# Optimization experiments

Measured on AMD Instinct MI355X. Metric: run time of the kernel, lower is better.

## Reference

```python
import math
import jax, jax.numpy as jnp
import numpy as np

N_HEADS = 16   # matches init_kwargs n_heads
C_SAMPLING = 1  # matches init_kwargs c_sampling


def setup_inputs() -> dict:
    rng = jax.random.key(0)
    ks = jax.random.split(rng, 8)
    L = S = 2048
    B = 8
    D = 1024
    sc = 0.02  # weight scale
    return {
        "query": jax.random.normal(ks[0], (L, B, D), jnp.float32),
        "key": jax.random.normal(ks[1], (S, B, D), jnp.float32),
        "value": jax.random.normal(ks[2], (S, B, D), jnp.float32),
        "Wq": jax.random.normal(ks[3], (D, D), jnp.float32) * sc,
        "bq": jnp.zeros((D,), jnp.float32),
        "Wk": jax.random.normal(ks[4], (D, D), jnp.float32) * sc,
        "bk": jnp.zeros((D,), jnp.float32),
        "Wv": jax.random.normal(ks[5], (D, D), jnp.float32) * sc,
        "bv": jnp.zeros((D,), jnp.float32),
        "Wo": jax.random.normal(ks[6], (D, D), jnp.float32) * sc,
        "bo": jnp.zeros((D,), jnp.float32),
    }


def _autocorr_forward(query, key, value, Wq, bq, Wk, bk, Wv, bv, Wo, bo):
    L, B, D = query.shape
    S = key.shape[0]
    H = N_HEADS
    E = D // H

    def proj(x, W, b):
        return x @ W.T + b

    def to_attn(x):  # (T,B,D) -> (B,H,E,T)
        T = x.shape[0]
        return x.reshape(T, B, H, E).transpose(1, 2, 3, 0)

    Q = to_attn(proj(query, Wq, bq))   # (B,H,E,L)
    K = to_attn(proj(key, Wk, bk))     # (B,H,E,S)
    V = to_attn(proj(value, Wv, bv))   # (B,H,E,S)

    # Align K/V length to L (static shapes: branch resolved at trace time)
    if L > S:
        pad = [(0, 0)] * 3 + [(0, L - S)]
        K = jnp.pad(K, pad)
        V = jnp.pad(V, pad)
    else:
        K = K[..., :L]
        V = V[..., :L]

    # Cross-correlation via FFT along time axis
    Qf = jnp.fft.rfft(Q, axis=-1)
    Kf = jnp.fft.rfft(K, axis=-1)
    corr = jnp.fft.irfft(Qf * jnp.conj(Kf), n=L, axis=-1)  # (B,H,E,L)

    # --- time_delay_agg ---
    topk = int(C_SAMPLING * math.log(L))
    mean_corr = corr.mean(axis=-2)                         # (B,H,L)
    scores, taus = jax.lax.top_k(mean_corr, topk)          # (B,H,topk)
    w = jax.nn.softmax(scores, axis=-1)                    # (B,H,topk)
    # delayed index (s + tau) mod L : (B,H,L,topk)
    idx = (jnp.arange(L)[None, None, :, None] + taus[:, :, None, :]) % L
    # gather V along time: (B,H,E,L,topk)
    delayed = jnp.take_along_axis(V[:, :, :, :, None], idx[:, :, None, :, :], axis=3)
    agg = jnp.mean(delayed * w[:, :, None, None, :], axis=-1)  # (B,H,E,L)

    # recover_from_attn: (B,H,E,L) -> (L,B,H*E)
    out = agg.transpose(3, 0, 1, 2).reshape(L, B, H * E)
    return out @ Wo.T + bo  # (L,B,D); need_weights=False so corr is dropped


def reference(query, key, value, Wq, bq, Wk, bk, Wv, bv, Wo, bo):
    return _autocorr_forward(query, key, value, Wq, bq, Wk, bk, Wv, bv, Wo, bo)
```

## Files before the change

### kernel.cpp

```cpp
#include <hip/hip_runtime.h>
#include <math.h>

#define TOPK 7

typedef __attribute__((ext_vector_type(8))) short bf16x8;
typedef __attribute__((ext_vector_type(4))) float f32x4;

__device__ __forceinline__ void glds16(const ushort* g, ushort* l)
{
    __builtin_amdgcn_global_load_lds(
        (const __attribute__((address_space(1))) void*)g,
        (__attribute__((address_space(3))) void*)l, 16, 0, 0);
}

__device__ __forceinline__ void split1(float x, ushort& h, ushort& lo)
{
    union U { float f; unsigned u; };
    U a; a.f = x;
    unsigned r = (a.u + 0x7FFFu + ((a.u >> 16) & 1u)) >> 16;
    h = (ushort)r;
    U b; b.u = r << 16;
    U d; d.f = x - b.f;
    unsigned r2 = (d.u + 0x7FFFu + ((d.u >> 16) & 1u)) >> 16;
    lo = (ushort)r2;
}

__global__ __launch_bounds__(256)
void split_f32(const float* __restrict__ x, ushort* __restrict__ hi,
               ushort* __restrict__ lo, int n4)
{
    for (int i = blockIdx.x * 256 + threadIdx.x; i < n4; i += gridDim.x * 256) {
        float4 v = ((const float4*)x)[i];
        ushort4 h, lw;
        split1(v.x, h.x, lw.x);
        split1(v.y, h.y, lw.y);
        split1(v.z, h.z, lw.z);
        split1(v.w, h.w, lw.w);
        ((ushort4*)hi)[i] = h;
        ((ushort4*)lo)[i] = lw;
    }
}

__global__ __launch_bounds__(256)
void wsplit4(const float* __restrict__ w0, const float* __restrict__ w1,
             const float* __restrict__ w2, const float* __restrict__ w3,
             ushort* __restrict__ o0, ushort* __restrict__ o1,
             ushort* __restrict__ o2, ushort* __restrict__ o3)
{
    const int m = blockIdx.x >> 10;
    const int lb = blockIdx.x & 1023;
    const float* src = (m == 0) ? w0 : (m == 1) ? w1 : (m == 2) ? w2 : w3;
    ushort* hi = (m == 0) ? o0 : (m == 1) ? o1 : (m == 2) ? o2 : o3;
    ushort* lo = hi + 1048576;
    const int n4 = 262144;
    for (int i = lb * 256 + threadIdx.x; i < n4; i += 1024 * 256) {
        float4 v = ((const float4*)src)[i];
        ushort4 h, lw;
        split1(v.x, h.x, lw.x);
        split1(v.y, h.y, lw.y);
        split1(v.z, h.z, lw.z);
        split1(v.w, h.w, lw.w);
        ((ushort4*)hi)[i] = h;
        ((ushort4*)lo)[i] = lw;
    }
}

template<bool TRANSP>
__global__ __launch_bounds__(512, 2)
void gemm_split(const ushort* __restrict__ Ah, const ushort* __restrict__ Al,
                const ushort* __restrict__ Bh, const ushort* __restrict__ Bl,
                const float* __restrict__ bias, float* __restrict__ C)
{
    __shared__ ushort lds[65536];
    const int tid = threadIdx.x;
    const int w = tid >> 6, l = tid & 63;

    const int ord = blockIdx.y * gridDim.x + blockIdx.x;
    const int cpx = (gridDim.x * gridDim.y) >> 3;
    const int swzb = (ord & 7) * cpx + (ord >> 3);
    const int bx = swzb & 3;
    const int by = swzb >> 2;

    const int wm = w >> 2, wn = w & 3;
    const int lr = l & 15, kgr = l >> 4;

    const ushort* gbB[4]; size_t goB[4]; int loB[4];
    const ushort* gbA[4]; size_t goA[4]; int loA[4];
#pragma unroll
    for (int q = 0; q < 4; ++q) {
        int idx = w * 4 + q;
        int cbq = idx >> 4;
        int kg = (idx >> 2) & 3;
        int rblk = idx & 3;
        gbB[q] = cbq ? Bl : Bh;
        goB[q] = (size_t)(bx * 256 + rblk * 64 + l) * 1024 + kg * 8;
        loB[q] = 16384 + cbq * 8192 + kg * 2048 + rblk * 512;
        gbA[q] = cbq ? Al : Ah;
        goA[q] = (size_t)(by * 256 + rblk * 64 + l) * 1024 + kg * 8;
        loA[q] = cbq * 8192 + kg * 2048 + rblk * 512;
    }

    f32x4 acc[8][4];
#pragma unroll
    for (int i = 0; i < 8; ++i)
#pragma unroll
        for (int j = 0; j < 4; ++j) acc[i][j] = (f32x4){0.f, 0.f, 0.f, 0.f};

#define STAGE_B(bufbase_, k0_) do { \
    const int _bb = (bufbase_); const int _kk = (k0_); \
    _Pragma("unroll") \
    for (int q = 0; q < 4; ++q) \
        glds16(gbB[q] + goB[q] + _kk, &lds[_bb + loB[q]]); \
} while (0)

#define STAGE_A2(bufbase_, k0_, qa_, qb_) do { \
    const int _bb = (bufbase_); const int _kk = (k0_); \
    glds16(gbA[qa_] + goA[qa_] + _kk, &lds[_bb + loA[qa_]]); \
    glds16(gbA[qb_] + goA[qb_] + _kk, &lds[_bb + loA[qb_]]); \
} while (0)

#define COMPUTE2(i0_) do { \
    _Pragma("unroll") \
    for (int ii = 0; ii < 2; ++ii) { \
        const int i = (i0_) + ii; \
        const int ra = wm * 128 + i * 16 + lr; \
        bf16x8 fah = *(const bf16x8*)&lb[       kgr * 2048 + ra * 8]; \
        bf16x8 fal = *(const bf16x8*)&lb[8192 + kgr * 2048 + ra * 8]; \
        __builtin_amdgcn_s_setprio(1); \
        _Pragma("unroll") \
        for (int j = 0; j < 4; ++j) \
            acc[i][j] = __builtin_amdgcn_mfma_f32_16x16x32_bf16(fah, fbh[j], acc[i][j], 0, 0, 0); \
        _Pragma("unroll") \
        for (int j = 0; j < 4; ++j) \
            acc[i][j] = __builtin_amdgcn_mfma_f32_16x16x32_bf16(fah, fbl[j], acc[i][j], 0, 0, 0); \
        _Pragma("unroll") \
        for (int j = 0; j < 4; ++j) \
            acc[i][j] = __builtin_amdgcn_mfma_f32_16x16x32_bf16(fal, fbh[j], acc[i][j], 0, 0, 0); \
        __builtin_amdgcn_s_setprio(0); \
    } \
} while (0)

    STAGE_B(0, 0);       STAGE_A2(0, 0, 0, 1);       STAGE_A2(0, 0, 2, 3);
    STAGE_B(32768, 32);  STAGE_A2(32768, 32, 0, 1);  STAGE_A2(32768, 32, 2, 3);
    asm volatile("s_waitcnt vmcnt(8)" ::: "memory");
    __builtin_amdgcn_s_barrier();

#pragma unroll 2
    for (int t = 0; t < 32; ++t) {
        const int cb = (t & 1) * 32768;
        const ushort* lb = &lds[cb];
        const bool pre = (t < 30);
        const int kn = (t + 2) * 32;

        bf16x8 fbh[4], fbl[4];
#pragma unroll
        for (int j = 0; j < 4; ++j) {
            int rb = wn * 64 + j * 16 + lr;
            fbh[j] = *(const bf16x8*)&lb[16384 + kgr * 2048 + rb * 8];
            fbl[j] = *(const bf16x8*)&lb[24576 + kgr * 2048 + rb * 8];
        }
        COMPUTE2(0);
        __builtin_amdgcn_s_barrier();

        if (pre) STAGE_B(cb, kn);
        COMPUTE2(2);
        __builtin_amdgcn_s_barrier();

        if (pre) STAGE_A2(cb, kn, 0, 2);
        COMPUTE2(4);
        __builtin_amdgcn_s_barrier();

        COMPUTE2(6);
        __builtin_amdgcn_s_barrier();
        if (pre) {
            STAGE_A2(cb, kn, 1, 3);
            asm volatile("s_waitcnt vmcnt(8)" ::: "memory");
        } else {
            asm volatile("s_waitcnt vmcnt(0)" ::: "memory");
        }
        __builtin_amdgcn_s_barrier();
    }
#undef STAGE_B
#undef STAGE_A2
#undef COMPUTE2

    if (!TRANSP) {
#pragma unroll
        for (int j = 0; j < 4; ++j) {
            int col = bx * 256 + wn * 64 + j * 16 + lr;
            float bb = bias[col];
#pragma unroll
            for (int i = 0; i < 8; ++i) {
                int row0 = by * 256 + wm * 128 + i * 16 + kgr * 4;
#pragma unroll
                for (int reg = 0; reg < 4; ++reg)
                    C[(size_t)(row0 + reg) * 1024 + col] = acc[i][j][reg] + bb;
            }
        }
    } else {
        float* lf = (float*)lds;
        const int e_r = (tid >> 3) & 63;
        const int tq = tid & 7;
#pragma unroll
        for (int ch = 0; ch < 2; ++ch) {
            __builtin_amdgcn_s_barrier();
            if ((wn >> 1) == ch) {
#pragma unroll
                for (int j = 0; j < 4; ++j) {
                    int col = bx * 256 + wn * 64 + j * 16 + lr;
                    float bb = bias[col];
                    int cl = (wn & 1) * 64 + j * 16 + lr;
#pragma unroll
                    for (int i = 0; i < 8; ++i) {
                        int rbase = wm * 128 + i * 16 + kgr * 4;
#pragma unroll
                        for (int reg = 0; reg < 4; ++reg) {
                            int rl = rbase + reg;
                            int cs = cl ^ ((rl >> 3) & 31);
                            lf[rl * 128 + cs] = acc[i][j][reg] + bb;
                        }
                    }
                }
            }
            __syncthreads();
#pragma unroll
            for (int it = 0; it < 16; ++it) {
                int b = it >> 1, hll = it & 1;
                float4 v;
#pragma unroll
                for (int k = 0; k < 4; ++k) {
                    int tl = tq * 4 + k;
                    int rl = tl * 8 + b;
                    int cs = (hll * 64 + e_r) ^ (tl & 31);
                    ((float*)&v)[k] = lf[rl * 128 + cs];
                }
                int bh = b * 16 + bx * 4 + ch * 2 + hll;
                ((float4*)C)[(size_t)(bh * 64 + e_r) * 512 + by * 8 + tq] = v;
            }
        }
    }
}

__global__ __launch_bounds__(256)
void transpose_bhet(const float* __restrict__ src, float* __restrict__ dst)
{
    __shared__ float tile[64][129];
    const int tid = threadIdx.x;
    const int bh = blockIdx.x;
    const int b = bh >> 4, h = bh & 15;
    const int t0 = blockIdx.y * 128;
    const float* sp = src + (size_t)(t0 * 8 + b) * 1024 + h * 64;
#pragma unroll
    for (int i = 0; i < 8; ++i) {
        int idx = i * 256 + tid;
        int t = idx >> 4;
        int e4 = (idx & 15) * 4;
        float4 v = *(const float4*)(sp + (size_t)t * 8192 + e4);
        tile[e4 + 0][t] = v.x; tile[e4 + 1][t] = v.y; tile[e4 + 2][t] = v.z; tile[e4 + 3][t] = v.w;
    }
    __syncthreads();
    float* dp = dst + (size_t)bh * 64 * 2048 + t0;
#pragma unroll
    for (int i = 0; i < 8; ++i) {
        int idx = i * 256 + tid;
        int e = idx >> 5;
        int t4 = (idx & 31) * 4;
        float4 o;
        o.x = tile[e][t4]; o.y = tile[e][t4 + 1]; o.z = tile[e][t4 + 2]; o.w = tile[e][t4 + 3];
        *(float4*)(dp + (size_t)e * 2048 + t4) = o;
    }
}

__device__ __forceinline__ float2 cadd(float2 a, float2 b){ return make_float2(a.x+b.x, a.y+b.y); }
__device__ __forceinline__ float2 csub(float2 a, float2 b){ return make_float2(a.x-b.x, a.y-b.y); }
__device__ __forceinline__ float2 cmul(float2 a, float2 b){ return make_float2(a.x*b.x - a.y*b.y, a.x*b.y + a.y*b.x); }

__device__ __forceinline__ int swz(int i) { return i ^ ((i >> 4) & 15); }

__device__ float2* fft2048(float2* x, float2* y, const float2* tw, int tid)
{
#pragma unroll 1
    for (int st = 0; st < 3; ++st) {
        const int s = 1 << (3 * st);
        const int u = tid;
        const int q = u & (s - 1);
        const int ps = u - q;
        float2 a = x[swz(u)],        e = x[swz(u + 256)];
        float2 b = x[swz(u + 512)],  f = x[swz(u + 768)];
        float2 c = x[swz(u + 1024)], g = x[swz(u + 1280)];
        float2 d = x[swz(u + 1536)], h = x[swz(u + 1792)];
        float2 t0 = cadd(a, c), t1 = csub(a, c);
        float2 t2 = cadd(b, d), tb = csub(b, d);
        float2 t3 = make_float2(tb.y, -tb.x);
        float2 A0 = cadd(t0, t2);
        float2 A1 = cmul(cadd(t1, t3), tw[ps]);
        float2 A2 = cmul(csub(t0, t2), tw[2 * ps]);
        float2 A3 = cmul(csub(t1, t3), tw[3 * ps]);
        float2 s0 = cadd(e, g), s1 = csub(e, g);
        float2 s2 = cadd(f, h), sb = csub(f, h);
        float2 s3 = make_float2(sb.y, -sb.x);
        float2 B0 = cadd(s0, s2);
        float2 B1 = cmul(cadd(s1, s3), tw[ps + 256]);
        float2 B2 = cmul(csub(s0, s2), tw[2 * ps + 512]);
        const int i3 = 3 * ps + 768;
        float2 w3b = (i3 < 1024) ? tw[i3]
                   : make_float2(-tw[i3 - 1024].x, -tw[i3 - 1024].y);
        float2 B3 = cmul(csub(s1, s3), w3b);
        float2 w4 = tw[4 * ps];
        const int o = 8 * ps + q;
        y[swz(o)]         = cadd(A0, B0);
        y[swz(o + s)]     = cadd(A1, B1);
        y[swz(o + 2 * s)] = cadd(A2, B2);
        y[swz(o + 3 * s)] = cadd(A3, B3);
        y[swz(o + 4 * s)] = cmul(csub(A0, B0), w4);
        y[swz(o + 5 * s)] = cmul(csub(A1, B1), w4);
        y[swz(o + 6 * s)] = cmul(csub(A2, B2), w4);
        y[swz(o + 7 * s)] = cmul(csub(A3, B3), w4);
        __syncthreads();
        float2* tsw = x; x = y; y = tsw;
    }
#pragma unroll
    for (int ui = 0; ui < 2; ++ui) {
        const int u = ui * 256 + tid;
        float2 a = x[swz(u)],        b = x[swz(u + 512)];
        float2 c = x[swz(u + 1024)], d = x[swz(u + 1536)];
        float2 t0 = cadd(a, c), t1 = csub(a, c);
        float2 t2 = cadd(b, d), tb = csub(b, d);
        float2 t3 = make_float2(tb.y, -tb.x);
        y[swz(u)]        = cadd(t0, t2);
        y[swz(u + 512)]  = cadd(t1, t3);
        y[swz(u + 1024)] = csub(t0, t2);
        y[swz(u + 1536)] = csub(t1, t3);
    }
    __syncthreads();
    return y;
}

__global__ __launch_bounds__(256)
void corr_fwd(const float* __restrict__ Qa, const float* __restrict__ Ka,
              float2* __restrict__ Spart)
{
    __shared__ float2 za[2048];
    __shared__ float2 zb[2048];
    __shared__ float2 tw[1024];
    const int tid = threadIdx.x;
    const int bh = blockIdx.x;
    const int eg = blockIdx.y;

#pragma unroll
    for (int r = 0; r < 4; ++r) {
        int u = tid + 256 * r;
        float sn, cs;
        sincospif((float)u * (1.0f / 1024.0f), &sn, &cs);
        tw[u] = make_float2(cs, -sn);
    }

    float2 sacc[4];
#pragma unroll
    for (int r = 0; r < 4; ++r) sacc[r] = make_float2(0.f, 0.f);
    float2 sacc1024 = make_float2(0.f, 0.f);

    const float* q0 = Qa + ((size_t)bh * 64 + eg * 8) * 2048;
    const float* k0 = Ka + ((size_t)bh * 64 + eg * 8) * 2048;

    for (int e = 0; e < 8; ++e) {
        const float* qr = q0 + (size_t)e * 2048;
        const float* kr = k0 + (size_t)e * 2048;
        for (int t = tid; t < 2048; t += 256)
            za[swz(t)] = make_float2(qr[t], kr[t]);
        __syncthreads();

        float2* res = fft2048(za, zb, tw, tid);

#pragma unroll
        for (int r = 0; r < 4; ++r) {
            int f = tid + 256 * r;
            float2 A  = res[swz(f)];
            float2 Bc = res[swz((2048 - f) & 2047)];
            float Ur = A.x + Bc.x, Ui = A.y - Bc.y;
            float Vr = A.x - Bc.x, Vi = -A.y - Bc.y;
            sacc[r].x += 0.25f * (-(Ur * Vi + Ui * Vr));
            sacc[r].y += 0.25f * ( Ur * Vr - Ui * Vi );
        }
        if (tid == 0) {
            float2 A = res[swz(1024)];
            float Ur = 2.f * A.x;
            float Vi = -2.f * A.y;
            sacc1024.x += 0.25f * (-(Ur * Vi));
            sacc1024.y += 0.25f * 0.f;
        }
        __syncthreads();
    }
    float2* sp = Spart + ((size_t)bh * 8 + eg) * 1025;
#pragma unroll
    for (int r = 0; r < 4; ++r) sp[tid + 256 * r] = sacc[r];
    if (tid == 0) sp[1024] = sacc1024;
}

__global__ __launch_bounds__(256)
void corr_inv_topk(const float2* __restrict__ Spart,
                   int* __restrict__ taus, float* __restrict__ wout)
{
    __shared__ float2 za[2048];
    __shared__ float2 zb[2048];
    __shared__ float2 tw[1024];
    __shared__ float2 Sh[1025];
    __shared__ float  redv[256];
    __shared__ int    redi[256];
    __shared__ float  sc[TOPK];
    __shared__ int    si[TOPK];

    const int tid = threadIdx.x;
    const int bh = blockIdx.x;

#pragma unroll
    for (int r = 0; r < 4; ++r) {
        int u = tid + 256 * r;
        float sn, cs;
        sincospif((float)u * (1.0f / 1024.0f), &sn, &cs);
        tw[u] = make_float2(cs, -sn);
    }

    const float2* sp0 = Spart + (size_t)bh * 8 * 1025;
    for (int f = tid; f < 1025; f += 256) {
        float2 s = make_float2(0.f, 0.f);
#pragma unroll
        for (int g = 0; g < 8; ++g) {
            float2 v = sp0[(size_t)g * 1025 + f];
            s.x += v.x; s.y += v.y;
        }
        Sh[f] = s;
    }
    __syncthreads();
    for (int f = tid; f < 2048; f += 256) {
        float2 v = (f <= 1024) ? make_float2(Sh[f].x, -Sh[f].y) : Sh[2048 - f];
        za[swz(f)] = v;
    }
    __syncthreads();

    float2* res = fft2048(za, zb, tw, tid);

    for (int k = 0; k < TOPK; ++k) {
        float bvv = -INFINITY; int bii = 0;
        for (int t = tid; t < 2048; t += 256) {
            float v = res[swz(t)].x;
            if (v > bvv) { bvv = v; bii = t; }
        }
        redv[tid] = bvv; redi[tid] = bii;
        __syncthreads();
        for (int off = 128; off > 0; off >>= 1) {
            if (tid < off) {
                float ov = redv[tid + off]; int oi = redi[tid + off];
                if (ov > redv[tid] || (ov == redv[tid] && oi < redi[tid])) { redv[tid] = ov; redi[tid] = oi; }
            }
            __syncthreads();
        }
        if (tid == 0) { sc[k] = redv[0]; si[k] = redi[0]; res[swz(redi[0])].x = -INFINITY; }
        __syncthreads();
    }
    if (tid == 0) {
        const float scale = 1.0f / (2048.0f * 64.0f);
        float m = sc[0] * scale;
        float ex[TOPK]; float ssum = 0.f;
        for (int k = 0; k < TOPK; ++k) { ex[k] = expf(sc[k] * scale - m); ssum += ex[k]; }
        for (int k = 0; k < TOPK; ++k) {
            taus[bh * TOPK + k] = si[k];
            wout[bh * TOPK + k] = ex[k] / ssum;
        }
    }
}

__global__ __launch_bounds__(256)
void agg_gather(const float* __restrict__ Vp, const int* __restrict__ taus,
                const float* __restrict__ w, ushort* __restrict__ ah,
                ushort* __restrict__ al)
{
    const int tid = threadIdx.x;
    const int bh = blockIdx.x;
    const int b = bh >> 4, h = bh & 15;
    const int t0 = blockIdx.y * 256;
    __shared__ int   stau[TOPK];
    __shared__ float sw[TOPK];
    if (tid < TOPK) { stau[tid] = taus[bh * TOPK + tid]; sw[tid] = w[bh * TOPK + tid] * (1.0f / TOPK); }
    __syncthreads();
    const float* vb = Vp + (size_t)b * 1024 + h * 64;
    ushort* ahb = ah + (size_t)b * 1024 + h * 64;
    ushort* alb = al + (size_t)b * 1024 + h * 64;
#pragma unroll
    for (int i = 0; i < 16; ++i) {
        int idx = i * 256 + tid;
        int t  = t0 + (idx >> 4);
        int e4 = (idx & 15) * 4;
        float a0 = 0.f, a1 = 0.f, a2 = 0.f, a3 = 0.f;
#pragma unroll
        for (int k = 0; k < TOPK; ++k) {
            int ts = (t + stau[k]) & 2047;
            float4 v = *(const float4*)(vb + (size_t)ts * 8192 + e4);
            a0 = fmaf(sw[k], v.x, a0); a1 = fmaf(sw[k], v.y, a1);
            a2 = fmaf(sw[k], v.z, a2); a3 = fmaf(sw[k], v.w, a3);
        }
        ushort4 hh, ll;
        split1(a0, hh.x, ll.x); split1(a1, hh.y, ll.y);
        split1(a2, hh.z, ll.z); split1(a3, hh.w, ll.w);
        *(ushort4*)(ahb + (size_t)t * 8192 + e4) = hh;
        *(ushort4*)(alb + (size_t)t * 8192 + e4) = ll;
    }
}

extern "C" void kernel_launch(void* const* d_in, const int* in_sizes, int n_in,
                              void* d_out, int out_size, void* d_ws, size_t ws_size,
                              hipStream_t stream)
{
    (void)in_sizes; (void)n_in; (void)out_size;
    const float* query = (const float*)d_in[0];
    const float* key   = (const float*)d_in[1];
    const float* value = (const float*)d_in[2];
    const float* Wq = (const float*)d_in[3];
    const float* bq = (const float*)d_in[4];
    const float* Wk = (const float*)d_in[5];
    const float* bk = (const float*)d_in[6];
    const float* Wv = (const float*)d_in[7];
    const float* bv = (const float*)d_in[8];
    const float* Wo = (const float*)d_in[9];
    const float* bo = (const float*)d_in[10];
    float* out = (float*)d_out;

    const size_t NEL  = (size_t)16777216;
    const size_t HEL  = NEL / 2;
    const size_t WEL  = (size_t)1048576;
    const size_t SLOTB = (size_t)64 * 1024 * 1024;
    const size_t MB = (size_t)1024 * 1024;

    char* ws = (char*)d_ws;
    float*  s1 = (float*)ws;
    char*   s2 = ws + SLOTB;
    char*   s3 = ws + 2 * SLOTB;
    char*   tail = ws + 3 * SLOTB;
    int*    dtaus = (int*)tail;
    float*  dw    = (float*)(dtaus + 128 * TOPK);
    const bool big_ws = ws_size >= 3 * SLOTB + (size_t)16 * MB;

    dim3 blk(256);
    dim3 gblk(512);
    dim3 gemm_full(4, 64), gemm_half(4, 32);
    dim3 tr_grid(128, 16);

    if (big_ws) {
        ushort* wqh = (ushort*)d_out;
        ushort* wkh = (ushort*)(tail + 4 * MB);
        ushort* wvh = (ushort*)(tail + 8 * MB);
        ushort* woh = (ushort*)(tail + 12 * MB);

        wsplit4<<<4096, blk, 0, stream>>>(Wq, Wk, Wv, Wo, wqh, wkh, wvh, woh);
        split_f32<<<2048, blk, 0, stream>>>(query, (ushort*)s2, (ushort*)s2 + NEL, (int)(NEL / 4));
        gemm_split<true><<<gemm_full, gblk, 0, stream>>>((ushort*)s2, (ushort*)s2 + NEL,
                                                         wqh, wqh + WEL, bq, (float*)s3);
        split_f32<<<2048, blk, 0, stream>>>(key, (ushort*)s2, (ushort*)s2 + NEL, (int)(NEL / 4));
        float* Ka = (float*)d_out;
        gemm_split<true><<<gemm_full, gblk, 0, stream>>>((ushort*)s2, (ushort*)s2 + NEL,
                                                         wkh, wkh + WEL, bk, Ka);
        split_f32<<<2048, blk, 0, stream>>>(value, (ushort*)s2, (ushort*)s2 + NEL, (int)(NEL / 4));
        gemm_split<false><<<gemm_full, gblk, 0, stream>>>((ushort*)s2, (ushort*)s2 + NEL,
                                                          wvh, wvh + WEL, bv, s1);
        float2* Spart = (float2*)s2;
        corr_fwd<<<dim3(128, 8), blk, 0, stream>>>((const float*)s3, Ka, Spart);
        corr_inv_topk<<<dim3(128), blk, 0, stream>>>(Spart, dtaus, dw);
        agg_gather<<<dim3(128, 8), blk, 0, stream>>>(s1, dtaus, dw,
                                                     (ushort*)s3, (ushort*)s3 + NEL);
        gemm_split<false><<<gemm_full, gblk, 0, stream>>>((ushort*)s3, (ushort*)s3 + NEL,
                                                          woh, woh + WEL, bo, out);
    } else {
        split_f32<<<1024, blk, 0, stream>>>(Wq, (ushort*)s3, (ushort*)s3 + WEL, (int)(WEL / 4));
        split_f32<<<2048, blk, 0, stream>>>(query, (ushort*)s2, (ushort*)s2 + NEL, (int)(NEL / 4));
        gemm_split<false><<<gemm_full, gblk, 0, stream>>>((ushort*)s2, (ushort*)s2 + NEL,
                                                          (ushort*)s3, (ushort*)s3 + WEL, bq, s1);
        transpose_bhet<<<tr_grid, blk, 0, stream>>>(s1, (float*)s2);
        ushort* wkh = (ushort*)d_out;
        split_f32<<<1024, blk, 0, stream>>>(Wk, wkh, wkh + WEL, (int)(WEL / 4));
        split_f32<<<2048, blk, 0, stream>>>(key, (ushort*)s3, (ushort*)s3 + NEL, (int)(NEL / 4));
        gemm_split<false><<<gemm_full, gblk, 0, stream>>>((ushort*)s3, (ushort*)s3 + NEL,
                                                          wkh, wkh + WEL, bk, s1);
        transpose_bhet<<<tr_grid, blk, 0, stream>>>(s1, (float*)s3);
        ushort* wvh = (ushort*)((char*)d_out + (size_t)32 * MB);
        split_f32<<<1024, blk, 0, stream>>>(Wv, wvh, wvh + WEL, (int)(WEL / 4));
        ushort* vsp = (ushort*)d_out;
        for (int hhalf = 0; hhalf < 2; ++hhalf) {
            split_f32<<<2048, blk, 0, stream>>>(value + hhalf * HEL, vsp, vsp + HEL, (int)(HEL / 4));
            gemm_split<false><<<gemm_half, gblk, 0, stream>>>(vsp, vsp + HEL, wvh, wvh + WEL,
                                                              bv, s1 + hhalf * HEL);
        }
        float2* Spart = (float2*)d_out;
        corr_fwd<<<dim3(128, 8), blk, 0, stream>>>((const float*)s2, (const float*)s3, Spart);
        corr_inv_topk<<<dim3(128), blk, 0, stream>>>(Spart, dtaus, dw);
        agg_gather<<<dim3(128, 8), blk, 0, stream>>>(s1, dtaus, dw,
                                                     (ushort*)s2, (ushort*)s2 + NEL);
        split_f32<<<1024, blk, 0, stream>>>(Wo, (ushort*)s3, (ushort*)s3 + WEL, (int)(WEL / 4));
        gemm_split<false><<<gemm_full, gblk, 0, stream>>>((ushort*)s2, (ushort*)s2 + NEL,
                                                          (ushort*)s3, (ushort*)s3 + WEL, bo, out);
    }
}
```

Measured before the change: 584.4 us.

## Shrink split-bf16 GEMM tile from 256x256 to 128x128 with 256-thread blocks

```diff
diff --git a/kernel.cpp b/kernel.cpp
--- a/kernel.cpp
+++ b/kernel.cpp
@@ -66,66 +66,63 @@
 }
 
 template<bool TRANSP>
-__global__ __launch_bounds__(512, 2)
+__global__ __launch_bounds__(256, 2)
 void gemm_split(const ushort* __restrict__ Ah, const ushort* __restrict__ Al,
                 const ushort* __restrict__ Bh, const ushort* __restrict__ Bl,
                 const float* __restrict__ bias, float* __restrict__ C)
 {
-    __shared__ ushort lds[65536];
+    __shared__ ushort lds[32768];
     const int tid = threadIdx.x;
     const int w = tid >> 6, l = tid & 63;
 
     const int ord = blockIdx.y * gridDim.x + blockIdx.x;
     const int cpx = (gridDim.x * gridDim.y) >> 3;
     const int swzb = (ord & 7) * cpx + (ord >> 3);
-    const int bx = swzb & 3;
-    const int by = swzb >> 2;
-
-    const int wm = w >> 2, wn = w & 3;
+    const int bx = swzb & 7;
+    const int by = swzb >> 3;
+
+    const int wm = w >> 1, wn = w & 1;
     const int lr = l & 15, kgr = l >> 4;
 
-    const ushort* gbB[4]; size_t goB[4]; int loB[4];
-    const ushort* gbA[4]; size_t goA[4]; int loA[4];
-#pragma unroll
-    for (int q = 0; q < 4; ++q) {
-        int idx = w * 4 + q;
-        int cbq = idx >> 4;
-        int kg = (idx >> 2) & 3;
-        int rblk = idx & 3;
-        gbB[q] = cbq ? Bl : Bh;
-        goB[q] = (size_t)(bx * 256 + rblk * 64 + l) * 1024 + kg * 8;
-        loB[q] = 16384 + cbq * 8192 + kg * 2048 + rblk * 512;
-        gbA[q] = cbq ? Al : Ah;
-        goA[q] = (size_t)(by * 256 + rblk * 64 + l) * 1024 + kg * 8;
-        loA[q] = cbq * 8192 + kg * 2048 + rblk * 512;
-    }
-
-    f32x4 acc[8][4];
-#pragma unroll
-    for (int i = 0; i < 8; ++i)
+    const ushort* gb[8]; size_t go[8]; int lof[8];
+#pragma unroll
+    for (int t = 0; t < 8; ++t) {
+        int comp = t >> 1;
+        int rblk = t & 1;
+        int kg = w;
+        int row0 = ((comp < 2) ? by : bx) * 128 + rblk * 64;
+        gb[t] = (comp == 0) ? Ah : (comp == 1) ? Al : (comp == 2) ? Bh : Bl;
+        go[t] = (size_t)(row0 + l) * 1024 + kg * 8;
+        lof[t] = comp * 4096 + kg * 1024 + rblk * 512;
+    }
+
+    f32x4 acc[4][4];
+#pragma unroll
+    for (int i = 0; i < 4; ++i)
 #pragma unroll
         for (int j = 0; j < 4; ++j) acc[i][j] = (f32x4){0.f, 0.f, 0.f, 0.f};
+
+#define STAGE_A(bufbase_, k0_) do { \
+    const int _bb = (bufbase_); const int _kk = (k0_); \
+    _Pragma("unroll") \
+    for (int st = 0; st < 4; ++st) \
+        glds16(gb[st] + go[st] + _kk, &lds[_bb + lof[st]]); \
+} while (0)
 
 #define STAGE_B(bufbase_, k0_) do { \
     const int _bb = (bufbase_); const int _kk = (k0_); \
     _Pragma("unroll") \
-    for (int q = 0; q < 4; ++q) \
-        glds16(gbB[q] + goB[q] + _kk, &lds[_bb + loB[q]]); \
-} while (0)
-
-#define STAGE_A2(bufbase_, k0_, qa_, qb_) do { \
-    const int _bb = (bufbase_); const int _kk = (k0_); \
-    glds16(gbA[qa_] + goA[qa_] + _kk, &lds[_bb + loA[qa_]]); \
-    glds16(gbA[qb_] + goA[qb_] + _kk, &lds[_bb + loA[qb_]]); \
+    for (int st = 4; st < 8; ++st) \
+        glds16(gb[st] + go[st] + _kk, &lds[_bb + lof[st]]); \
 } while (0)
 
 #define COMPUTE2(i0_) do { \
     _Pragma("unroll") \
     for (int ii = 0; ii < 2; ++ii) { \
         const int i = (i0_) + ii; \
-        const int ra = wm * 128 + i * 16 + lr; \
-        bf16x8 fah = *(const bf16x8*)&lb[       kgr * 2048 + ra * 8]; \
-        bf16x8 fal = *(const bf16x8*)&lb[8192 + kgr * 2048 + ra * 8]; \
+        const int ra = wm * 64 + i * 16 + lr; \
+        bf16x8 fah = *(const bf16x8*)&lb[       kgr * 1024 + ra * 8]; \
+        bf16x8 fal = *(const bf16x8*)&lb[4096 + kgr * 1024 + ra * 8]; \
         __builtin_amdgcn_s_setprio(1); \
         _Pragma("unroll") \
         for (int j = 0; j < 4; ++j) \
@@ -140,14 +137,14 @@
     } \
 } while (0)
 
-    STAGE_B(0, 0);       STAGE_A2(0, 0, 0, 1);       STAGE_A2(0, 0, 2, 3);
-    STAGE_B(32768, 32);  STAGE_A2(32768, 32, 0, 1);  STAGE_A2(32768, 32, 2, 3);
+    STAGE_B(0, 0);      STAGE_A(0, 0);
+    STAGE_B(16384, 32); STAGE_A(16384, 32);
     asm volatile("s_waitcnt vmcnt(8)" ::: "memory");
     __builtin_amdgcn_s_barrier();
 
 #pragma unroll 2
     for (int t = 0; t < 32; ++t) {
-        const int cb = (t & 1) * 32768;
+        const int cb = (t & 1) * 16384;
         const ushort* lb = &lds[cb];
         const bool pre = (t < 30);
         const int kn = (t + 2) * 32;
@@ -156,8 +153,8 @@
 #pragma unroll
         for (int j = 0; j < 4; ++j) {
             int rb = wn * 64 + j * 16 + lr;
-            fbh[j] = *(const bf16x8*)&lb[16384 + kgr * 2048 + rb * 8];
-            fbl[j] = *(const bf16x8*)&lb[24576 + kgr * 2048 + rb * 8];
+            fbh[j] = *(const bf16x8*)&lb[8192  + kgr * 1024 + rb * 8];
+            fbl[j] = *(const bf16x8*)&lb[12288 + kgr * 1024 + rb * 8];
         }
         COMPUTE2(0);
         __builtin_amdgcn_s_barrier();
@@ -166,32 +163,26 @@
         COMPUTE2(2);
         __builtin_amdgcn_s_barrier();
 
-        if (pre) STAGE_A2(cb, kn, 0, 2);
-        COMPUTE2(4);
-        __builtin_amdgcn_s_barrier();
-
-        COMPUTE2(6);
-        __builtin_amdgcn_s_barrier();
         if (pre) {
-            STAGE_A2(cb, kn, 1, 3);
+            STAGE_A(cb, kn);
             asm volatile("s_waitcnt vmcnt(8)" ::: "memory");
         } else {
             asm volatile("s_waitcnt vmcnt(0)" ::: "memory");
         }
         __builtin_amdgcn_s_barrier();
     }
+#undef STAGE_A
 #undef STAGE_B
-#undef STAGE_A2
 #undef COMPUTE2
 
     if (!TRANSP) {
 #pragma unroll
         for (int j = 0; j < 4; ++j) {
-            int col = bx * 256 + wn * 64 + j * 16 + lr;
+            int col = bx * 128 + wn * 64 + j * 16 + lr;
             float bb = bias[col];
 #pragma unroll
-            for (int i = 0; i < 8; ++i) {
-                int row0 = by * 256 + wm * 128 + i * 16 + kgr * 4;
+            for (int i = 0; i < 4; ++i) {
+                int row0 = by * 128 + wm * 64 + i * 16 + kgr * 4;
 #pragma unroll
                 for (int reg = 0; reg < 4; ++reg)
                     C[(size_t)(row0 + reg) * 1024 + col] = acc[i][j][reg] + bb;
@@ -199,44 +190,38 @@
         }
     } else {
         float* lf = (float*)lds;
-        const int e_r = (tid >> 3) & 63;
-        const int tq = tid & 7;
-#pragma unroll
-        for (int ch = 0; ch < 2; ++ch) {
-            __builtin_amdgcn_s_barrier();
-            if ((wn >> 1) == ch) {
-#pragma unroll
-                for (int j = 0; j < 4; ++j) {
-                    int col = bx * 256 + wn * 64 + j * 16 + lr;
-                    float bb = bias[col];
-                    int cl = (wn & 1) * 64 + j * 16 + lr;
-#pragma unroll
-                    for (int i = 0; i < 8; ++i) {
-                        int rbase = wm * 128 + i * 16 + kgr * 4;
-#pragma unroll
-                        for (int reg = 0; reg < 4; ++reg) {
-                            int rl = rbase + reg;
-                            int cs = cl ^ ((rl >> 3) & 31);
-                            lf[rl * 128 + cs] = acc[i][j][reg] + bb;
-                        }
-                    }
+#pragma unroll
+        for (int j = 0; j < 4; ++j) {
+            int col = bx * 128 + wn * 64 + j * 16 + lr;
+            float bb = bias[col];
+            int cl = wn * 64 + j * 16 + lr;
+#pragma unroll
+            for (int i = 0; i < 4; ++i) {
+                int rbase = wm * 64 + i * 16 + kgr * 4;
+#pragma unroll
+                for (int reg = 0; reg < 4; ++reg) {
+                    int rl = rbase + reg;
+                    lf[rl * 128 + (cl ^ (rl & 31))] = acc[i][j][reg] + bb;
                 }
             }
-            __syncthreads();
-#pragma unroll
-            for (int it = 0; it < 16; ++it) {
-                int b = it >> 1, hll = it & 1;
-                float4 v;
-#pragma unroll
-                for (int k = 0; k < 4; ++k) {
-                    int tl = tq * 4 + k;
-                    int rl = tl * 8 + b;
-                    int cs = (hll * 64 + e_r) ^ (tl & 31);
-                    ((float*)&v)[k] = lf[rl * 128 + cs];
-                }
-                int bh = b * 16 + bx * 4 + ch * 2 + hll;
-                ((float4*)C)[(size_t)(bh * 64 + e_r) * 512 + by * 8 + tq] = v;
+        }
+        __syncthreads();
+#pragma unroll
+        for (int it = 0; it < 16; ++it) {
+            int vi = it * 256 + tid;
+            int tq4 = vi & 3;
+            int e   = (vi >> 2) & 63;
+            int hll = (vi >> 8) & 1;
+            int b   = vi >> 9;
+            float4 v;
+#pragma unroll
+            for (int k = 0; k < 4; ++k) {
+                int rl = (tq4 * 4 + k) * 8 + b;
+                int cl = hll * 64 + e;
+                ((float*)&v)[k] = lf[rl * 128 + (cl ^ (rl & 31))];
             }
+            int bh = b * 16 + bx * 2 + hll;
+            ((float4*)C)[(size_t)(bh * 64 + e) * 512 + by * 4 + tq4] = v;
         }
     }
 }
@@ -541,8 +526,7 @@
     const bool big_ws = ws_size >= 3 * SLOTB + (size_t)16 * MB;
 
     dim3 blk(256);
-    dim3 gblk(512);
-    dim3 gemm_full(4, 64), gemm_half(4, 32);
+    dim3 gemm_full(8, 128), gemm_half(8, 64);
     dim3 tr_grid(128, 16);
 
     if (big_ws) {
@@ -553,41 +537,41 @@
 
         wsplit4<<<4096, blk, 0, stream>>>(Wq, Wk, Wv, Wo, wqh, wkh, wvh, woh);
         split_f32<<<2048, blk, 0, stream>>>(query, (ushort*)s2, (ushort*)s2 + NEL, (int)(NEL / 4));
-        gemm_split<true><<<gemm_full, gblk, 0, stream>>>((ushort*)s2, (ushort*)s2 + NEL,
-                                                         wqh, wqh + WEL, bq, (float*)s3);
+        gemm_split<true><<<gemm_full, blk, 0, stream>>>((ushort*)s2, (ushort*)s2 + NEL,
+                                                        wqh, wqh + WEL, bq, (float*)s3);
         split_f32<<<2048, blk, 0, stream>>>(key, (ushort*)s2, (ushort*)s2 + NEL, (int)(NEL / 4));
         float* Ka = (float*)d_out;
-        gemm_split<true><<<gemm_full, gblk, 0, stream>>>((ushort*)s2, (ushort*)s2 + NEL,
-                                                         wkh, wkh + WEL, bk, Ka);
+        gemm_split<true><<<gemm_full, blk, 0, stream>>>((ushort*)s2, (ushort*)s2 + NEL,
+                                                        wkh, wkh + WEL, bk, Ka);
         split_f32<<<2048, blk, 0, stream>>>(value, (ushort*)s2, (ushort*)s2 + NEL, (int)(NEL / 4));
-        gemm_split<false><<<gemm_full, gblk, 0, stream>>>((ushort*)s2, (ushort*)s2 + NEL,
-                                                          wvh, wvh + WEL, bv, s1);
+        gemm_split<false><<<gemm_full, blk, 0, stream>>>((ushort*)s2, (ushort*)s2 + NEL,
+                                                         wvh, wvh + WEL, bv, s1);
         float2* Spart = (float2*)s2;
         corr_fwd<<<dim3(128, 8), blk, 0, stream>>>((const float*)s3, Ka, Spart);
         corr_inv_topk<<<dim3(128), blk, 0, stream>>>(Spart, dtaus, dw);
         agg_gather<<<dim3(128, 8), blk, 0, stream>>>(s1, dtaus, dw,
                                                      (ushort*)s3, (ushort*)s3 + NEL);
-        gemm_split<false><<<gemm_full, gblk, 0, stream>>>((ushort*)s3, (ushort*)s3 + NEL,
-                                                          woh, woh + WEL, bo, out);
+        gemm_split<false><<<gemm_full, blk, 0, stream>>>((ushort*)s3, (ushort*)s3 + NEL,
+                                                         woh, woh + WEL, bo, out);
     } else {
         split_f32<<<1024, blk, 0, stream>>>(Wq, (ushort*)s3, (ushort*)s3 + WEL, (int)(WEL / 4));
         split_f32<<<2048, blk, 0, stream>>>(query, (ushort*)s2, (ushort*)s2 + NEL, (int)(NEL / 4));
-        gemm_split<false><<<gemm_full, gblk, 0, stream>>>((ushort*)s2, (ushort*)s2 + NEL,
-                                                          (ushort*)s3, (ushort*)s3 + WEL, bq, s1);
+        gemm_split<false><<<gemm_full, blk, 0, stream>>>((ushort*)s2, (ushort*)s2 + NEL,
+                                                         (ushort*)s3, (ushort*)s3 + WEL, bq, s1);
         transpose_bhet<<<tr_grid, blk, 0, stream>>>(s1, (float*)s2);
         ushort* wkh = (ushort*)d_out;
         split_f32<<<1024, blk, 0, stream>>>(Wk, wkh, wkh + WEL, (int)(WEL / 4));
         split_f32<<<2048, blk, 0, stream>>>(key, (ushort*)s3, (ushort*)s3 + NEL, (int)(NEL / 4));
-        gemm_split<false><<<gemm_full, gblk, 0, stream>>>((ushort*)s3, (ushort*)s3 + NEL,
-                                                          wkh, wkh + WEL, bk, s1);
+        gemm_split<false><<<gemm_full, blk, 0, stream>>>((ushort*)s3, (ushort*)s3 + NEL,
+                                                         wkh, wkh + WEL, bk, s1);
         transpose_bhet<<<tr_grid, blk, 0, stream>>>(s1, (float*)s3);
         ushort* wvh = (ushort*)((char*)d_out + (size_t)32 * MB);
         split_f32<<<1024, blk, 0, stream>>>(Wv, wvh, wvh + WEL, (int)(WEL / 4));
         ushort* vsp = (ushort*)d_out;
         for (int hhalf = 0; hhalf < 2; ++hhalf) {
             split_f32<<<2048, blk, 0, stream>>>(value + hhalf * HEL, vsp, vsp + HEL, (int)(HEL / 4));
-            gemm_split<false><<<gemm_half, gblk, 0, stream>>>(vsp, vsp + HEL, wvh, wvh + WEL,
-                                                              bv, s1 + hhalf * HEL);
+            gemm_split<false><<<gemm_half, blk, 0, stream>>>(vsp, vsp + HEL, wvh, wvh + WEL,
+                                                             bv, s1 + hhalf * HEL);
         }
         float2* Spart = (float2*)d_out;
         corr_fwd<<<dim3(128, 8), blk, 0, stream>>>((const float*)s2, (const float*)s3, Spart);
@@ -595,7 +579,7 @@
         agg_gather<<<dim3(128, 8), blk, 0, stream>>>(s1, dtaus, dw,
                                                      (ushort*)s2, (ushort*)s2 + NEL);
         split_f32<<<1024, blk, 0, stream>>>(Wo, (ushort*)s3, (ushort*)s3 + WEL, (int)(WEL / 4));
-        gemm_split<false><<<gemm_full, gblk, 0, stream>>>((ushort*)s2, (ushort*)s2 + NEL,
-                                                          (ushort*)s3, (ushort*)s3 + WEL, bo, out);
-    }
-}
+        gemm_split<false><<<gemm_full, blk, 0, stream>>>((ushort*)s2, (ushort*)s2 + NEL,
+                                                         (ushort*)s3, (ushort*)s3 + WEL, bo, out);
+    }
+}
```

After: 719.4 us. 23.1% more time.

## Single-buffer GEMM LDS to raise occupancy to four blocks per CU

Applied to the files above, without the earlier changes.

```diff
diff --git a/kernel.cpp b/kernel.cpp
--- a/kernel.cpp
+++ b/kernel.cpp
@@ -66,12 +66,12 @@
 }
 
 template<bool TRANSP>
-__global__ __launch_bounds__(512, 2)
+__global__ __launch_bounds__(512, 4)
 void gemm_split(const ushort* __restrict__ Ah, const ushort* __restrict__ Al,
                 const ushort* __restrict__ Bh, const ushort* __restrict__ Bl,
                 const float* __restrict__ bias, float* __restrict__ C)
 {
-    __shared__ ushort lds[65536];
+    __shared__ ushort lds[32768];
     const int tid = threadIdx.x;
     const int w = tid >> 6, l = tid & 63;
 
@@ -106,17 +106,17 @@
 #pragma unroll
         for (int j = 0; j < 4; ++j) acc[i][j] = (f32x4){0.f, 0.f, 0.f, 0.f};
 
-#define STAGE_B(bufbase_, k0_) do { \
-    const int _bb = (bufbase_); const int _kk = (k0_); \
+#define STAGE_B(k0_) do { \
+    const int _kk = (k0_); \
     _Pragma("unroll") \
     for (int q = 0; q < 4; ++q) \
-        glds16(gbB[q] + goB[q] + _kk, &lds[_bb + loB[q]]); \
+        glds16(gbB[q] + goB[q] + _kk, &lds[loB[q]]); \
 } while (0)
 
-#define STAGE_A2(bufbase_, k0_, qa_, qb_) do { \
-    const int _bb = (bufbase_); const int _kk = (k0_); \
-    glds16(gbA[qa_] + goA[qa_] + _kk, &lds[_bb + loA[qa_]]); \
-    glds16(gbA[qb_] + goA[qb_] + _kk, &lds[_bb + loA[qb_]]); \
+#define STAGE_A2(k0_, qa_, qb_) do { \
+    const int _kk = (k0_); \
+    glds16(gbA[qa_] + goA[qa_] + _kk, &lds[loA[qa_]]); \
+    glds16(gbA[qb_] + goA[qb_] + _kk, &lds[loA[qb_]]); \
 } while (0)
 
 #define COMPUTE2(i0_) do { \
@@ -124,8 +124,8 @@
     for (int ii = 0; ii < 2; ++ii) { \
         const int i = (i0_) + ii; \
         const int ra = wm * 128 + i * 16 + lr; \
-        bf16x8 fah = *(const bf16x8*)&lb[       kgr * 2048 + ra * 8]; \
-        bf16x8 fal = *(const bf16x8*)&lb[8192 + kgr * 2048 + ra * 8]; \
+        bf16x8 fah = *(const bf16x8*)&lds[       kgr * 2048 + ra * 8]; \
+        bf16x8 fal = *(const bf16x8*)&lds[8192 + kgr * 2048 + ra * 8]; \
         __builtin_amdgcn_s_setprio(1); \
         _Pragma("unroll") \
         for (int j = 0; j < 4; ++j) \
@@ -140,41 +140,43 @@
     } \
 } while (0)
 
-    STAGE_B(0, 0);       STAGE_A2(0, 0, 0, 1);       STAGE_A2(0, 0, 2, 3);
-    STAGE_B(32768, 32);  STAGE_A2(32768, 32, 0, 1);  STAGE_A2(32768, 32, 2, 3);
-    asm volatile("s_waitcnt vmcnt(8)" ::: "memory");
+    STAGE_B(0); STAGE_A2(0, 0, 2); STAGE_A2(0, 1, 3);
+    asm volatile("s_waitcnt vmcnt(0)" ::: "memory");
     __builtin_amdgcn_s_barrier();
 
 #pragma unroll 2
     for (int t = 0; t < 32; ++t) {
-        const int cb = (t & 1) * 32768;
-        const ushort* lb = &lds[cb];
-        const bool pre = (t < 30);
-        const int kn = (t + 2) * 32;
+        const bool pre = (t < 31);
+        const int kn = (t + 1) * 32;
 
         bf16x8 fbh[4], fbl[4];
 #pragma unroll
         for (int j = 0; j < 4; ++j) {
             int rb = wn * 64 + j * 16 + lr;
-            fbh[j] = *(const bf16x8*)&lb[16384 + kgr * 2048 + rb * 8];
-            fbl[j] = *(const bf16x8*)&lb[24576 + kgr * 2048 + rb * 8];
+            fbh[j] = *(const bf16x8*)&lds[16384 + kgr * 2048 + rb * 8];
+            fbl[j] = *(const bf16x8*)&lds[24576 + kgr * 2048 + rb * 8];
         }
         COMPUTE2(0);
         __builtin_amdgcn_s_barrier();
 
-        if (pre) STAGE_B(cb, kn);
+        if (pre) STAGE_B(kn);
         COMPUTE2(2);
+        if (pre) {
+            asm volatile("s_waitcnt vmcnt(4)" ::: "memory");
+        } else {
+            asm volatile("s_waitcnt vmcnt(0)" ::: "memory");
+        }
         __builtin_amdgcn_s_barrier();
 
-        if (pre) STAGE_A2(cb, kn, 0, 2);
+        if (pre) STAGE_A2(kn, 0, 2);
         COMPUTE2(4);
         __builtin_amdgcn_s_barrier();
 
         COMPUTE2(6);
         __builtin_amdgcn_s_barrier();
         if (pre) {
-            STAGE_A2(cb, kn, 1, 3);
-            asm volatile("s_waitcnt vmcnt(8)" ::: "memory");
+            STAGE_A2(kn, 1, 3);
+            asm volatile("s_waitcnt vmcnt(2)" ::: "memory");
         } else {
             asm volatile("s_waitcnt vmcnt(0)" ::: "memory");
         }
@@ -199,43 +201,41 @@
         }
     } else {
         float* lf = (float*)lds;
-        const int e_r = (tid >> 3) & 63;
-        const int tq = tid & 7;
-#pragma unroll
-        for (int ch = 0; ch < 2; ++ch) {
-            __builtin_amdgcn_s_barrier();
-            if ((wn >> 1) == ch) {
+#pragma unroll
+        for (int p = 0; p < 4; ++p) {
+            __syncthreads();
+            if (wn == p) {
 #pragma unroll
                 for (int j = 0; j < 4; ++j) {
                     int col = bx * 256 + wn * 64 + j * 16 + lr;
                     float bb = bias[col];
-                    int cl = (wn & 1) * 64 + j * 16 + lr;
+                    int cl = j * 16 + lr;
 #pragma unroll
                     for (int i = 0; i < 8; ++i) {
                         int rbase = wm * 128 + i * 16 + kgr * 4;
 #pragma unroll
                         for (int reg = 0; reg < 4; ++reg) {
                             int rl = rbase + reg;
-                            int cs = cl ^ ((rl >> 3) & 31);
-                            lf[rl * 128 + cs] = acc[i][j][reg] + bb;
+                            lf[rl * 64 + (cl ^ (rl & 31))] = acc[i][j][reg] + bb;
                         }
                     }
                 }
             }
             __syncthreads();
 #pragma unroll
-            for (int it = 0; it < 16; ++it) {
-                int b = it >> 1, hll = it & 1;
+            for (int it = 0; it < 8; ++it) {
+                int vi = it * 512 + tid;
+                int tq = vi & 7;
+                int e  = (vi >> 3) & 63;
+                int b  = vi >> 9;
                 float4 v;
 #pragma unroll
                 for (int k = 0; k < 4; ++k) {
-                    int tl = tq * 4 + k;
-                    int rl = tl * 8 + b;
-                    int cs = (hll * 64 + e_r) ^ (tl & 31);
-                    ((float*)&v)[k] = lf[rl * 128 + cs];
+                    int rl = (tq * 4 + k) * 8 + b;
+                    ((float*)&v)[k] = lf[rl * 64 + (e ^ (rl & 31))];
                 }
-                int bh = b * 16 + bx * 4 + ch * 2 + hll;
-                ((float4*)C)[(size_t)(bh * 64 + e_r) * 512 + by * 8 + tq] = v;
+                int bh = b * 16 + bx * 4 + p;
+                ((float4*)C)[(size_t)(bh * 64 + e) * 512 + by * 8 + tq] = v;
             }
         }
     }
```

Measured after the change: 2.279 ms. 3.9x slower.
